# Kernel optimization log

Hardware: AMD Instinct MI355X
Metric: run time of the kernel (lower is better)

## Reference

```python
import jax, jax.numpy as jnp
import numpy as np

T, B, D, K = 256, 128, 1024, 21
PAD = 0


def setup_inputs() -> dict:
    key = jax.random.key(0)
    k1, k2, k3, k4, k5, k6, k7 = jax.random.split(key, 7)
    lstm_features = jax.random.normal(k1, (T, B, D), dtype=jnp.float32)
    # gold tags: non-pad (1..K-1) for a random prefix, PAD afterwards; mask[0] all on
    tags = jax.random.randint(k2, (T, B), 1, K)
    lengths = jax.random.randint(k3, (B,), T // 2, T + 1)
    tags = jnp.where(jnp.arange(T)[:, None] < lengths[None, :], tags, PAD)
    W = jax.random.normal(k4, (D, K), dtype=jnp.float32) * 0.02
    b = jnp.zeros((K,), dtype=jnp.float32)
    # torchcrf initializes transitions uniform(-0.1, 0.1)
    start_transitions = jax.random.uniform(k5, (K,), minval=-0.1, maxval=0.1)
    end_transitions = jax.random.uniform(k6, (K,), minval=-0.1, maxval=0.1)
    transitions = jax.random.uniform(k7, (K, K), minval=-0.1, maxval=0.1)
    return {
        'lstm_features': lstm_features,
        'tags': tags,
        'W': W,
        'b': b,
        'start_transitions': start_transitions,
        'end_transitions': end_transitions,
        'transitions': transitions,
    }


def _crf_nll(emissions, tags, mask, start, end, trans):
    # emissions: (T,B,K), tags/mask: (T,B). Returns -sum_b log p(tags|emissions)
    maskf = mask.astype(emissions.dtype)
    # --- numerator: score of gold path (fully vectorized over t) ---
    em_score = jnp.take_along_axis(emissions, tags[:, :, None], axis=2)[:, :, 0]  # (T,B)
    tr_score = trans[tags[:-1], tags[1:]]                                          # (T-1,B)
    num = start[tags[0]] + em_score[0]
    num = num + jnp.sum((tr_score + em_score[1:]) * maskf[1:], axis=0)
    seq_ends = jnp.sum(mask.astype(jnp.int32), axis=0) - 1                         # (B,)
    last_tags = jnp.take_along_axis(tags, seq_ends[None, :], axis=0)[0]
    num = num + end[last_tags]
    # --- denominator: forward algorithm (log partition) via scan ---
    def step(score, xs):  # score: (B,K)
        emit_t, mask_t = xs
        nxt = jax.nn.logsumexp(score[:, :, None] + trans[None, :, :] + emit_t[:, None, :], axis=1)
        return jnp.where(mask_t[:, None], nxt, score), None
    score0 = start[None, :] + emissions[0]
    scoreT, _ = jax.lax.scan(step, score0, (emissions[1:], mask[1:]))
    den = jax.nn.logsumexp(scoreT + end[None, :], axis=1)                          # (B,)
    return -jnp.sum(num - den)


def _viterbi(emissions, mask, start, end, trans):
    # returns best tag sequence (T,B) int32, padded positions set to PAD
    n_tags = emissions.shape[-1]
    ident = jnp.arange(n_tags, dtype=jnp.int32)[None, :]
    def step(score, xs):  # score: (B,K)
        emit_t, mask_t = xs
        cand = score[:, :, None] + trans[None, :, :]          # (B, prev K, next K)
        best_prev = jnp.argmax(cand, axis=1).astype(jnp.int32)  # (B,K)
        nxt = jnp.max(cand, axis=1) + emit_t
        ptr = jnp.where(mask_t[:, None], best_prev, ident)    # identity ptr on padding
        new_score = jnp.where(mask_t[:, None], nxt, score)
        return new_score, ptr
    score0 = start[None, :] + emissions[0]
    scoreT, history = jax.lax.scan(step, score0, (emissions[1:], mask[1:]))  # history: (T-1,B,K)
    last_tag = jnp.argmax(scoreT + end[None, :], axis=1).astype(jnp.int32)   # (B,)
    def back(tag, hist_t):
        prev = jnp.take_along_axis(hist_t, tag[:, None], axis=1)[:, 0]
        return prev, tag
    first_tag, rest = jax.lax.scan(back, last_tag, history, reverse=True)    # rest = tags[1:]
    best = jnp.concatenate([first_tag[None, :], rest], axis=0)               # (T,B)
    return jnp.where(mask, best, PAD)


def reference(lstm_features, tags, W, b, start_transitions, end_transitions, transitions):
    # Linear projection; dropout is identity at inference
    fc_out = jnp.einsum('tbd,dk->tbk', lstm_features, W) + b
    mask = tags != PAD
    crf_out = _viterbi(fc_out, mask, start_transitions, end_transitions, transitions)
    crf_loss = _crf_nll(fc_out, tags, mask, start_transitions, end_transitions, transitions)
    return crf_out, crf_loss
```

## Files before the change

### kernel.cpp

```cpp
#include <hip/hip_runtime.h>
#include <math.h>

#define T_ 256
#define B_ 128
#define D_ 1024
#define K_ 21
#define NB3 43

typedef short v8s __attribute__((ext_vector_type(8)));
typedef float v4f __attribute__((ext_vector_type(4)));

__device__ __forceinline__ short bf16rne(float f) {
  unsigned u = __float_as_uint(f);
  u += 0x7FFFu + ((u >> 16) & 1u);
  return (short)(u >> 16);
}
__device__ __forceinline__ float rdl(float v, int l) {
  return __int_as_float(__builtin_amdgcn_readlane(__float_as_int(v), l));
}

__global__ __launch_bounds__(256) void fc_kernel(
    const float* __restrict__ A, const float* __restrict__ W,
    const float* __restrict__ bias, float* __restrict__ fc) {
  __shared__ float red[3][64][22];
  const int lane = threadIdx.x & 63;
  const int wv = threadIdx.x >> 6;
  const int m15 = lane & 15, g4 = lane >> 4;
  const int rowbase = blockIdx.x * 64;
  const int kc = wv * 256;
  const int n1 = 16 + m15;

  v8s bf[8][2];
#pragma unroll
  for (int s = 0; s < 8; ++s) {
    const float* Wp = W + (size_t)(kc + 32 * s + 8 * g4) * K_;
#pragma unroll
    for (int j = 0; j < 8; ++j) bf[s][0][j] = bf16rne(Wp[j * K_ + m15]);
    if (n1 < K_) {
#pragma unroll
      for (int j = 0; j < 8; ++j) bf[s][1][j] = bf16rne(Wp[j * K_ + n1]);
    } else {
#pragma unroll
      for (int j = 0; j < 8; ++j) bf[s][1][j] = 0;
    }
  }

  v4f acc[4][2];
#pragma unroll
  for (int m = 0; m < 4; ++m) {
    acc[m][0] = (v4f)(0.f);
    acc[m][1] = (v4f)(0.f);
  }

#pragma unroll
  for (int s = 0; s < 8; ++s) {
    v8s av[4];
#pragma unroll
    for (int m = 0; m < 4; ++m) {
      const float* Ap =
          A + (size_t)(rowbase + 16 * m + m15) * D_ + kc + 32 * s + 8 * g4;
      const float4 x = *(const float4*)Ap;
      const float4 y = *(const float4*)(Ap + 4);
      av[m][0] = bf16rne(x.x); av[m][1] = bf16rne(x.y);
      av[m][2] = bf16rne(x.z); av[m][3] = bf16rne(x.w);
      av[m][4] = bf16rne(y.x); av[m][5] = bf16rne(y.y);
      av[m][6] = bf16rne(y.z); av[m][7] = bf16rne(y.w);
    }
#pragma unroll
    for (int m = 0; m < 4; ++m) {
      acc[m][0] = __builtin_amdgcn_mfma_f32_16x16x32_bf16(av[m], bf[s][0],
                                                          acc[m][0], 0, 0, 0);
      acc[m][1] = __builtin_amdgcn_mfma_f32_16x16x32_bf16(av[m], bf[s][1],
                                                          acc[m][1], 0, 0, 0);
    }
  }

  if (wv > 0) {
#pragma unroll
    for (int m = 0; m < 4; ++m)
#pragma unroll
      for (int ri = 0; ri < 4; ++ri) {
        const int rl = 16 * m + 4 * g4 + ri;
        red[wv - 1][rl][m15] = acc[m][0][ri];
        if (n1 < K_) red[wv - 1][rl][n1] = acc[m][1][ri];
      }
  }
  __syncthreads();
  if (wv == 0) {
    const float b0 = bias[m15];
    const float b1 = (n1 < K_) ? bias[n1] : 0.f;
#pragma unroll
    for (int m = 0; m < 4; ++m)
#pragma unroll
      for (int ri = 0; ri < 4; ++ri) {
        const int rl = 16 * m + 4 * g4 + ri;
        float* o = fc + (size_t)(rowbase + rl) * K_;
        o[m15] = acc[m][0][ri] + red[0][rl][m15] + red[1][rl][m15] +
                 red[2][rl][m15] + b0;
        if (n1 < K_)
          o[n1] = acc[m][1][ri] + red[0][rl][n1] + red[1][rl][n1] +
                  red[2][rl][n1] + b1;
      }
  }
}

__global__ __launch_bounds__(64) void scan_kernel(
    const float* __restrict__ fc, const int* __restrict__ tags,
    const float* __restrict__ startT, const float* __restrict__ endT,
    const float* __restrict__ trans, float* __restrict__ out_tags,
    float* __restrict__ out_loss) {
  __shared__ unsigned short bp[256 * 66];
  __shared__ unsigned char h2[127 * 66];
  __shared__ unsigned char h4[63 * 66];
  __shared__ unsigned char cur[3 * 256];
  __shared__ v4f statev[18];

  const int lane = threadIdx.x;
  const int blk = blockIdx.x;

  if (blk < 2 * NB3) {
    const bool fwd = blk < NB3;
    const int bblk = fwd ? blk : blk - NB3;
    int g = lane / 21;
    if (g > 2) g = 2;
    int jloc = lane - g * 21;
    if (jloc > 20) jloc = 20;
    int batch = bblk * 3 + g;
    if (batch >= B_) batch = B_ - 1;

    int len0 = 0, len1 = 0, len2 = 0;
#pragma unroll
    for (int q = 0; q < 4; ++q) {
      const int t = q * 64 + lane;
      int b0 = bblk * 3, b1 = bblk * 3 + 1, b2 = bblk * 3 + 2;
      if (b1 >= B_) b1 = B_ - 1;
      if (b2 >= B_) b2 = B_ - 1;
      len0 += __popcll(__ballot(tags[t * B_ + b0] != 0));
      len1 += __popcll(__ballot(tags[t * B_ + b1] != 0));
      len2 += __popcll(__ballot(tags[t * B_ + b2] != 0));
    }
    const int mylen = (g == 0) ? len0 : (g == 1) ? len1 : len2;

    float* sb = (float*)statev + g * 24;
    const v4f* sv = (const v4f*)sb;
    const float em0 = fc[(size_t)batch * K_ + jloc];

    if (fwd) {
      float ec[21];
#pragma unroll
      for (int i = 0; i < K_; ++i) ec[i] = __expf(trans[i * K_ + jloc]);
      float p = __expf(startT[jloc] + em0);
      sb[jloc] = p;
      float L = 0.f;
      float vt1 = fc[((size_t)1 * B_ + batch) * K_ + jloc];
      float vt2 = fc[((size_t)2 * B_ + batch) * K_ + jloc];
      float ee = __expf(vt1);

      for (int t = 1; t < T_; ++t) {
        const v4f A0 = sv[0], A1 = sv[1], A2 = sv[2], A3 = sv[3], A4 = sv[4];
        const float A5 = sb[20];
        const float eet = ee;
        ee = __expf(vt2);
        const int tn = (t + 2 < T_) ? t + 2 : T_ - 1;
        vt2 = fc[((size_t)tn * B_ + batch) * K_ + jloc];

        float d0 = A0[0] * ec[0], d1 = A0[1] * ec[1], d2 = A0[2] * ec[2];
        d0 = fmaf(A0[3], ec[3], d0); d1 = fmaf(A1[0], ec[4], d1); d2 = fmaf(A1[1], ec[5], d2);
        d0 = fmaf(A1[2], ec[6], d0); d1 = fmaf(A1[3], ec[7], d1); d2 = fmaf(A2[0], ec[8], d2);
        d0 = fmaf(A2[1], ec[9], d0); d1 = fmaf(A2[2], ec[10], d1); d2 = fmaf(A2[3], ec[11], d2);
        d0 = fmaf(A3[0], ec[12], d0); d1 = fmaf(A3[1], ec[13], d1); d2 = fmaf(A3[2], ec[14], d2);
        d0 = fmaf(A3[3], ec[15], d0); d1 = fmaf(A4[0], ec[16], d1); d2 = fmaf(A4[1], ec[17], d2);
        d0 = fmaf(A4[2], ec[18], d0); d1 = fmaf(A4[3], ec[19], d1); d2 = fmaf(A5, ec[20], d2);

        const float pn = ((d0 + d1) + d2) * eet;
        p = (t < mylen) ? pn : p;
        if ((t & 7) == 0) {
          const float f = A0[0];
          p *= __builtin_amdgcn_rcpf(f);
          L += __logf(f);
        }
        sb[jloc] = p;
      }
      const float w = p * __expf(endT[jloc]);
      float res = 0.f;
#pragma unroll
      for (int gg = 0; gg < 3; ++gg) {
        if (bblk * 3 + gg < B_) {
          float tot = 0.f;
#pragma unroll
          for (int i = 0; i < K_; ++i) tot += rdl(w, gg * K_ + i);
          res += rdl(L, gg * K_) + __logf(tot);
        }
      }
      if (lane == 0) atomicAdd(out_loss, res);
    } else {
      float tr[21];
#pragma unroll
      for (int i = 0; i < K_; ++i) tr[i] = trans[i * K_ + jloc] + 2048.0f;
      float sc = startT[jloc] + em0;
      sb[jloc] = sc;
      float vt1 = fc[((size_t)1 * B_ + batch) * K_ + jloc];
      float vt2 = fc[((size_t)2 * B_ + batch) * K_ + jloc];

      for (int t = 1; t < T_; ++t) {
        const v4f A0 = sv[0], A1 = sv[1], A2 = sv[2], A3 = sv[3], A4 = sv[4];
        const float A5 = sb[20];
        const float emt = vt1;
        vt1 = vt2;
        const int tn = (t + 2 < T_) ? t + 2 : T_ - 1;
        vt2 = fc[((size_t)tn * B_ + batch) * K_ + jloc];

        int k0 = 0, k1 = 0, k2 = 0;
#define VT(i, V)                                                             \
        {                                                                    \
          const float c = (V) + tr[i];                                       \
          const int kk = (__float_as_int(c) & 0xFFFFFFE0) | (20 - (i));      \
          if ((i) % 3 == 0) k0 = k0 > kk ? k0 : kk;                          \
          else if ((i) % 3 == 1) k1 = k1 > kk ? k1 : kk;                     \
          else k2 = k2 > kk ? k2 : kk;                                       \
        }
        VT(0, A0[0]) VT(1, A0[1]) VT(2, A0[2]) VT(3, A0[3])
        VT(4, A1[0]) VT(5, A1[1]) VT(6, A1[2]) VT(7, A1[3])
        VT(8, A2[0]) VT(9, A2[1]) VT(10, A2[2]) VT(11, A2[3])
        VT(12, A3[0]) VT(13, A3[1]) VT(14, A3[2]) VT(15, A3[3])
        VT(16, A4[0]) VT(17, A4[1]) VT(18, A4[2]) VT(19, A4[3])
        VT(20, A5)
#undef VT
        int km = k0 > k1 ? k0 : k1;
        km = km > k2 ? km : k2;
        const float nxt = __int_as_float(km & 0xFFFFFFE0) - 2048.0f + emt;
        const bool m = t < mylen;
        sc = m ? nxt : sc;
        sb[jloc] = sc;
        const int pw = m ? (20 - (km & 31)) : jloc;
        if (lane < 63) bp[t * 66 + g * 22 + jloc] = (unsigned short)pw;
      }
      __syncthreads();

      const float finb = sc + endT[jloc] + 2048.0f;
      const int myk = (__float_as_int(finb) & 0xFFFFFFE0) | (20 - jloc);
      int last0 = 0, last1 = 0, last2 = 0;
#pragma unroll
      for (int gg = 0; gg < 3; ++gg) {
        int km = 0;
#pragma unroll
        for (int i = 0; i < K_; ++i) {
          const int ki = __builtin_amdgcn_readlane(myk, gg * K_ + i);
          km = km > ki ? km : ki;
        }
        const int lt = 20 - (km & 31);
        if (gg == 0) last0 = lt;
        else if (gg == 1) last1 = lt;
        else last2 = lt;
      }

      for (int i = lane; i < 127 * 63; i += 64) {
        const int v = i / 63;
        const int rem = i - v * 63;
        const int gg = rem / 21, j = rem - (rem / 21) * 21;
        h2[v * 66 + gg * 22 + j] = (unsigned char)
            bp[(2 * v + 1) * 66 + gg * 22 + bp[(2 * v + 2) * 66 + gg * 22 + j]];
      }
      __syncthreads();
      for (int i = lane; i < 63 * 63; i += 64) {
        const int w = i / 63;
        const int rem = i - w * 63;
        const int gg = rem / 21, j = rem - (rem / 21) * 21;
        h4[w * 66 + gg * 22 + j] =
            h2[(2 * w) * 66 + gg * 22 + h2[(2 * w + 1) * 66 + gg * 22 + j]];
      }
      __syncthreads();

      if (lane < 3 && bblk * 3 + lane < B_) {
        int c = (lane == 0) ? last0 : (lane == 1) ? last1 : last2;
        cur[lane * 256 + 255] = (unsigned char)c;
        c = bp[255 * 66 + lane * 22 + c];
        cur[lane * 256 + 254] = (unsigned char)c;
        c = h2[126 * 66 + lane * 22 + c];
        cur[lane * 256 + 252] = (unsigned char)c;
        for (int w = 62; w >= 0; --w) {
          c = h4[w * 66 + lane * 22 + c];
          cur[lane * 256 + 4 * w] = (unsigned char)c;
        }
      }
      __syncthreads();
      for (int i = lane; i < 63 * 3; i += 64) {
        const int gg = i / 63, ii = i - (i / 63) * 63;
        const int t = 2 + 4 * ii;
        cur[gg * 256 + t] =
            h2[(t >> 1) * 66 + gg * 22 + cur[gg * 256 + t + 2]];
      }
      __syncthreads();
      for (int i = lane; i < 127 * 3; i += 64) {
        const int gg = i / 127, ii = i - (i / 127) * 127;
        const int t = 1 + 2 * ii;
        cur[gg * 256 + t] = (unsigned char)
            bp[(t + 1) * 66 + gg * 22 + cur[gg * 256 + t + 1]];
      }
      __syncthreads();
      for (int i = lane; i < 3 * 256; i += 64) {
        const int gg = i >> 8, t = i & 255;
        const int bb = bblk * 3 + gg;
        const int lg = (gg == 0) ? len0 : (gg == 1) ? len1 : len2;
        if (bb < B_)
          out_tags[t * B_ + bb] = (t < lg) ? (float)cur[gg * 256 + t] : 0.f;
      }
    }
  } else {
    const int b = blk - 2 * NB3;
    float contrib = 0.f;
#pragma unroll
    for (int q = 0; q < 4; ++q) {
      const int t = lane * 4 + q;
      const int tg = tags[t * B_ + b];
      const size_t ro = ((size_t)t * B_ + b) * K_;
      if (t == 0) {
        contrib += startT[tg] + fc[ro + tg];
      } else if (tg != 0) {
        const int pg = tags[(t - 1) * B_ + b];
        contrib += trans[pg * K_ + tg] + fc[ro + tg];
      }
      const bool isLast =
          (tg != 0) && (t == T_ - 1 || tags[(t + 1) * B_ + b] == 0);
      if (isLast) contrib += endT[tg];
    }
#pragma unroll
    for (int off = 32; off > 0; off >>= 1)
      contrib += __shfl_down(contrib, off, 64);
    if (lane == 0) atomicAdd(out_loss, -contrib);
  }
}

extern "C" void kernel_launch(void* const* d_in, const int* in_sizes, int n_in,
                              void* d_out, int out_size, void* d_ws,
                              size_t ws_size, hipStream_t stream) {
  const float* A = (const float*)d_in[0];
  const int* tags = (const int*)d_in[1];
  const float* W = (const float*)d_in[2];
  const float* bias = (const float*)d_in[3];
  const float* startT = (const float*)d_in[4];
  const float* endT = (const float*)d_in[5];
  const float* trans = (const float*)d_in[6];

  float* out_tags = (float*)d_out;
  float* out_loss = (float*)d_out + (size_t)T_ * B_;
  float* fc = (float*)d_ws;

  hipMemsetAsync(out_loss, 0, sizeof(float), stream);
  fc_kernel<<<512, 256, 0, stream>>>(A, W, bias, fc);
  scan_kernel<<<2 * NB3 + B_, 64, 0, stream>>>(fc, tags, startT, endT, trans,
                                               out_tags, out_loss);
}
```

Baseline: 298.1 us.

## Stage emissions into LDS via async global_load_lds double buffer in scan

The forward and Viterbi scan loops now prefetch 32-timestep chunks of emissions for the block's three batches into a double-buffered LDS tile using global_load_lds, in place of per-step global loads issued two steps ahead. The intent is to take global memory latency off the serial recurrence's critical path. The Viterbi max reduction is also rebuilt as a tree of 3-way integer maxes to shorten the dependency chain. The hipMemset for the loss is folded into fc_kernel to save one launch. The chunked loads read 64 floats per row, which spans slightly past the three batches, and each chunk boundary adds a vmcnt wait.

```diff
diff --git a/kernel.cpp b/kernel.cpp
--- a/kernel.cpp
+++ b/kernel.cpp
@@ -18,11 +18,23 @@
 __device__ __forceinline__ float rdl(float v, int l) {
   return __int_as_float(__builtin_amdgcn_readlane(__float_as_int(v), l));
 }
+__device__ __forceinline__ int imax3(int a, int b, int c) {
+  const int t = a > b ? a : b;
+  return t > c ? t : c;
+}
+
+typedef const __attribute__((address_space(1))) void* gas1_t;
+typedef __attribute__((address_space(3))) void* las3_t;
+__device__ __forceinline__ void gload_lds(const float* g, float* l) {
+  __builtin_amdgcn_global_load_lds((gas1_t)g, (las3_t)l, 4, 0, 0);
+}
 
 __global__ __launch_bounds__(256) void fc_kernel(
     const float* __restrict__ A, const float* __restrict__ W,
-    const float* __restrict__ bias, float* __restrict__ fc) {
+    const float* __restrict__ bias, float* __restrict__ fc,
+    float* __restrict__ out_loss) {
   __shared__ float red[3][64][22];
+  if (blockIdx.x == 0 && threadIdx.x == 0) *out_loss = 0.f;
   const int lane = threadIdx.x & 63;
   const int wv = threadIdx.x >> 6;
   const int m15 = lane & 15, g4 = lane >> 4;
@@ -109,11 +121,12 @@
     const float* __restrict__ startT, const float* __restrict__ endT,
     const float* __restrict__ trans, float* __restrict__ out_tags,
     float* __restrict__ out_loss) {
+  __shared__ v4f statev[18];
+  __shared__ float fcs[2][32][64];
   __shared__ unsigned short bp[256 * 66];
   __shared__ unsigned char h2[127 * 66];
   __shared__ unsigned char h4[63 * 66];
   __shared__ unsigned char cur[3 * 256];
-  __shared__ v4f statev[18];
 
   const int lane = threadIdx.x;
   const int blk = blockIdx.x;
@@ -125,25 +138,43 @@
     if (g > 2) g = 2;
     int jloc = lane - g * 21;
     if (jloc > 20) jloc = 20;
-    int batch = bblk * 3 + g;
-    if (batch >= B_) batch = B_ - 1;
+    const int gj = g * 21 + jloc;
+    const int b0 = bblk * 3;
 
     int len0 = 0, len1 = 0, len2 = 0;
 #pragma unroll
     for (int q = 0; q < 4; ++q) {
       const int t = q * 64 + lane;
-      int b0 = bblk * 3, b1 = bblk * 3 + 1, b2 = bblk * 3 + 2;
-      if (b1 >= B_) b1 = B_ - 1;
-      if (b2 >= B_) b2 = B_ - 1;
-      len0 += __popcll(__ballot(tags[t * B_ + b0] != 0));
-      len1 += __popcll(__ballot(tags[t * B_ + b1] != 0));
-      len2 += __popcll(__ballot(tags[t * B_ + b2] != 0));
+      int bb0 = b0, bb1 = b0 + 1, bb2 = b0 + 2;
+      if (bb1 >= B_) bb1 = B_ - 1;
+      if (bb2 >= B_) bb2 = B_ - 1;
+      len0 += __popcll(__ballot(tags[t * B_ + bb0] != 0));
+      len1 += __popcll(__ballot(tags[t * B_ + bb1] != 0));
+      len2 += __popcll(__ballot(tags[t * B_ + bb2] != 0));
     }
     const int mylen = (g == 0) ? len0 : (g == 1) ? len1 : len2;
 
     float* sb = (float*)statev + g * 24;
     const v4f* sv = (const v4f*)sb;
-    const float em0 = fc[(size_t)batch * K_ + jloc];
+
+#define STAGE(c)                                                             \
+    {                                                                        \
+      const float* src_ = fc + ((size_t)((c) * 32) * B_ + b0) * K_ + lane;   \
+      float* dst_ = &fcs[(c) & 1][0][0];                                     \
+      _Pragma("unroll")                                                      \
+      for (int q_ = 0; q_ < 32; ++q_)                                        \
+        gload_lds(src_ + (size_t)q_ * (B_ * K_), dst_ + q_ * 64);            \
+    }
+#define WAIT_VM0()                                                           \
+    {                                                                        \
+      asm volatile("s_waitcnt vmcnt(0)" ::: "memory");                       \
+      __builtin_amdgcn_sched_barrier(0);                                     \
+    }
+
+    STAGE(0)
+    WAIT_VM0()
+    const float em0 = fcs[0][0][gj];
+    STAGE(1)
 
     if (fwd) {
       float ec[21];
@@ -152,40 +183,50 @@
       float p = __expf(startT[jloc] + em0);
       sb[jloc] = p;
       float L = 0.f;
-      float vt1 = fc[((size_t)1 * B_ + batch) * K_ + jloc];
-      float vt2 = fc[((size_t)2 * B_ + batch) * K_ + jloc];
-      float ee = __expf(vt1);
-
-      for (int t = 1; t < T_; ++t) {
-        const v4f A0 = sv[0], A1 = sv[1], A2 = sv[2], A3 = sv[3], A4 = sv[4];
-        const float A5 = sb[20];
-        const float eet = ee;
-        ee = __expf(vt2);
-        const int tn = (t + 2 < T_) ? t + 2 : T_ - 1;
-        vt2 = fc[((size_t)tn * B_ + batch) * K_ + jloc];
-
-        float d0 = A0[0] * ec[0], d1 = A0[1] * ec[1], d2 = A0[2] * ec[2];
-        d0 = fmaf(A0[3], ec[3], d0); d1 = fmaf(A1[0], ec[4], d1); d2 = fmaf(A1[1], ec[5], d2);
-        d0 = fmaf(A1[2], ec[6], d0); d1 = fmaf(A1[3], ec[7], d1); d2 = fmaf(A2[0], ec[8], d2);
-        d0 = fmaf(A2[1], ec[9], d0); d1 = fmaf(A2[2], ec[10], d1); d2 = fmaf(A2[3], ec[11], d2);
-        d0 = fmaf(A3[0], ec[12], d0); d1 = fmaf(A3[1], ec[13], d1); d2 = fmaf(A3[2], ec[14], d2);
-        d0 = fmaf(A3[3], ec[15], d0); d1 = fmaf(A4[0], ec[16], d1); d2 = fmaf(A4[1], ec[17], d2);
-        d0 = fmaf(A4[2], ec[18], d0); d1 = fmaf(A4[3], ec[19], d1); d2 = fmaf(A5, ec[20], d2);
-
-        const float pn = ((d0 + d1) + d2) * eet;
-        p = (t < mylen) ? pn : p;
-        if ((t & 7) == 0) {
-          const float f = A0[0];
-          p *= __builtin_amdgcn_rcpf(f);
-          L += __logf(f);
-        }
-        sb[jloc] = p;
-      }
+
+      for (int c = 0; c < 8; ++c) {
+        const float* fb = &fcs[c & 1][0][0];
+        const int t1 = c * 32 + 32;
+        for (int t = c ? c * 32 : 1; t < t1; ++t) {
+          const float emt = fb[(t & 31) * 64 + gj];
+          const v4f A0 = sv[0], A1 = sv[1], A2 = sv[2], A3 = sv[3],
+                    A4 = sv[4];
+          const float A5 = sb[20];
+
+          float d0 = A0[0] * ec[0], d1 = A0[1] * ec[1], d2 = A0[2] * ec[2];
+          d0 = fmaf(A0[3], ec[3], d0); d1 = fmaf(A1[0], ec[4], d1);
+          d2 = fmaf(A1[1], ec[5], d2);
+          d0 = fmaf(A1[2], ec[6], d0); d1 = fmaf(A1[3], ec[7], d1);
+          d2 = fmaf(A2[0], ec[8], d2);
+          d0 = fmaf(A2[1], ec[9], d0); d1 = fmaf(A2[2], ec[10], d1);
+          d2 = fmaf(A2[3], ec[11], d2);
+          d0 = fmaf(A3[0], ec[12], d0); d1 = fmaf(A3[1], ec[13], d1);
+          d2 = fmaf(A3[2], ec[14], d2);
+          d0 = fmaf(A3[3], ec[15], d0); d1 = fmaf(A4[0], ec[16], d1);
+          d2 = fmaf(A4[1], ec[17], d2);
+          d0 = fmaf(A4[2], ec[18], d0); d1 = fmaf(A4[3], ec[19], d1);
+          d2 = fmaf(A5, ec[20], d2);
+
+          const float pn = ((d0 + d1) + d2) * __expf(emt);
+          p = (t < mylen) ? pn : p;
+          if ((t & 7) == 0) {
+            const float f = A0[0];
+            p *= __builtin_amdgcn_rcpf(f);
+            L += __logf(f);
+          }
+          sb[jloc] = p;
+        }
+        if (c < 7) {
+          WAIT_VM0()
+          if (c + 2 < 8) STAGE(c + 2)
+        }
+      }
+
       const float w = p * __expf(endT[jloc]);
       float res = 0.f;
 #pragma unroll
       for (int gg = 0; gg < 3; ++gg) {
-        if (bblk * 3 + gg < B_) {
+        if (b0 + gg < B_) {
           float tot = 0.f;
 #pragma unroll
           for (int i = 0; i < K_; ++i) tot += rdl(w, gg * K_ + i);
@@ -199,41 +240,37 @@
       for (int i = 0; i < K_; ++i) tr[i] = trans[i * K_ + jloc] + 2048.0f;
       float sc = startT[jloc] + em0;
       sb[jloc] = sc;
-      float vt1 = fc[((size_t)1 * B_ + batch) * K_ + jloc];
-      float vt2 = fc[((size_t)2 * B_ + batch) * K_ + jloc];
-
-      for (int t = 1; t < T_; ++t) {
-        const v4f A0 = sv[0], A1 = sv[1], A2 = sv[2], A3 = sv[3], A4 = sv[4];
-        const float A5 = sb[20];
-        const float emt = vt1;
-        vt1 = vt2;
-        const int tn = (t + 2 < T_) ? t + 2 : T_ - 1;
-        vt2 = fc[((size_t)tn * B_ + batch) * K_ + jloc];
-
-        int k0 = 0, k1 = 0, k2 = 0;
-#define VT(i, V)                                                             \
-        {                                                                    \
-          const float c = (V) + tr[i];                                       \
-          const int kk = (__float_as_int(c) & 0xFFFFFFE0) | (20 - (i));      \
-          if ((i) % 3 == 0) k0 = k0 > kk ? k0 : kk;                          \
-          else if ((i) % 3 == 1) k1 = k1 > kk ? k1 : kk;                     \
-          else k2 = k2 > kk ? k2 : kk;                                       \
-        }
-        VT(0, A0[0]) VT(1, A0[1]) VT(2, A0[2]) VT(3, A0[3])
-        VT(4, A1[0]) VT(5, A1[1]) VT(6, A1[2]) VT(7, A1[3])
-        VT(8, A2[0]) VT(9, A2[1]) VT(10, A2[2]) VT(11, A2[3])
-        VT(12, A3[0]) VT(13, A3[1]) VT(14, A3[2]) VT(15, A3[3])
-        VT(16, A4[0]) VT(17, A4[1]) VT(18, A4[2]) VT(19, A4[3])
-        VT(20, A5)
-#undef VT
-        int km = k0 > k1 ? k0 : k1;
-        km = km > k2 ? km : k2;
-        const float nxt = __int_as_float(km & 0xFFFFFFE0) - 2048.0f + emt;
-        const bool m = t < mylen;
-        sc = m ? nxt : sc;
-        sb[jloc] = sc;
-        const int pw = m ? (20 - (km & 31)) : jloc;
-        if (lane < 63) bp[t * 66 + g * 22 + jloc] = (unsigned short)pw;
+
+      for (int c = 0; c < 8; ++c) {
+        const float* fb = &fcs[c & 1][0][0];
+        const int t1 = c * 32 + 32;
+        for (int t = c ? c * 32 : 1; t < t1; ++t) {
+          const float emt = fb[(t & 31) * 64 + gj];
+          const v4f A0 = sv[0], A1 = sv[1], A2 = sv[2], A3 = sv[3],
+                    A4 = sv[4];
+          const float A5 = sb[20];
+
+#define KEY(i, V) ((__float_as_int((V) + tr[i]) & 0xFFFFFFE0) | (20 - (i)))
+          const int q0 = imax3(KEY(0, A0[0]), KEY(1, A0[1]), KEY(2, A0[2]));
+          const int q1 = imax3(KEY(3, A0[3]), KEY(4, A1[0]), KEY(5, A1[1]));
+          const int q2 = imax3(KEY(6, A1[2]), KEY(7, A1[3]), KEY(8, A2[0]));
+          const int q3 = imax3(KEY(9, A2[1]), KEY(10, A2[2]), KEY(11, A2[3]));
+          const int q4 = imax3(KEY(12, A3[0]), KEY(13, A3[1]), KEY(14, A3[2]));
+          const int q5 = imax3(KEY(15, A3[3]), KEY(16, A4[0]), KEY(17, A4[1]));
+          const int q6 = imax3(KEY(18, A4[2]), KEY(19, A4[3]), KEY(20, A5));
+          const int km = imax3(imax3(q0, q1, q2), imax3(q3, q4, q5), q6);
+#undef KEY
+          const float nxt = __int_as_float(km & 0xFFFFFFE0) - 2048.0f + emt;
+          const bool m = t < mylen;
+          sc = m ? nxt : sc;
+          sb[jloc] = sc;
+          const int pw = m ? (20 - (km & 31)) : jloc;
+          bp[t * 66 + g * 22 + jloc] = (unsigned short)pw;
+        }
+        if (c < 7) {
+          WAIT_VM0()
+          if (c + 2 < 8) STAGE(c + 2)
+        }
       }
       __syncthreads();
 
@@ -271,7 +308,7 @@
       }
       __syncthreads();
 
-      if (lane < 3 && bblk * 3 + lane < B_) {
+      if (lane < 3 && b0 + lane < B_) {
         int c = (lane == 0) ? last0 : (lane == 1) ? last1 : last2;
         cur[lane * 256 + 255] = (unsigned char)c;
         c = bp[255 * 66 + lane * 22 + c];
@@ -300,12 +337,14 @@
       __syncthreads();
       for (int i = lane; i < 3 * 256; i += 64) {
         const int gg = i >> 8, t = i & 255;
-        const int bb = bblk * 3 + gg;
+        const int bb = b0 + gg;
         const int lg = (gg == 0) ? len0 : (gg == 1) ? len1 : len2;
         if (bb < B_)
           out_tags[t * B_ + bb] = (t < lg) ? (float)cur[gg * 256 + t] : 0.f;
       }
     }
+#undef STAGE
+#undef WAIT_VM0
   } else {
     const int b = blk - 2 * NB3;
     float contrib = 0.f;
@@ -346,8 +385,7 @@
   float* out_loss = (float*)d_out + (size_t)T_ * B_;
   float* fc = (float*)d_ws;
 
-  hipMemsetAsync(out_loss, 0, sizeof(float), stream);
-  fc_kernel<<<512, 256, 0, stream>>>(A, W, bias, fc);
+  fc_kernel<<<512, 256, 0, stream>>>(A, W, bias, fc, out_loss);
   scan_kernel<<<2 * NB3 + B_, 64, 0, stream>>>(fc, tags, startT, endT, trans,
                                                out_tags, out_loss);
 }
```

Result: faster. 280.8 us (-5.8%).
